# Performance work log

Measured on AMD Instinct MI355X. Metric: run time of the kernel, lower is better.

Reference implementation:

```python
import jax, jax.numpy as jnp
import numpy as np

B, C, L = 2, 2, 20
D = H = W = 160


def setup_inputs() -> dict:
    key = jax.random.key(0)
    k1, k2, k3, k4 = jax.random.split(key, 4)
    labels = jax.random.randint(k1, (B, 1, D, H, W), 0, L, dtype=jnp.int32)
    means = jax.random.normal(k2, (B, L, C), dtype=jnp.float32)
    stds = jax.random.uniform(k3, (B, L, C), dtype=jnp.float32)
    # noise is sampled once per (b, c) volume in the original module
    noise = jax.random.normal(k4, (B, C, D, H, W), dtype=jnp.float32)
    gen_labels = jnp.arange(L, dtype=jnp.int32)  # generation_labels (sorted)
    return {"labels": labels, "means": means, "stds": stds,
            "noise": noise, "gen_labels": gen_labels}


def reference(labels, means, stds, noise, gen_labels):
    Bb, _, Dd, Hh, Ww = labels.shape
    Cc = means.shape[-1]
    Ll = gen_labels.shape[0]
    lab = labels[:, 0].reshape(Bb, -1)                      # [B, V]
    # map label value -> index into generation_labels (sorted)
    idx = jnp.searchsorted(gen_labels, lab)                 # [B, V]
    idx = jnp.clip(idx, 0, Ll - 1)
    valid = gen_labels[idx] == lab                          # labels not in set stay 0
    m = jnp.take_along_axis(means, idx[:, :, None], axis=1)  # [B, V, C]
    s = jnp.take_along_axis(stds, idx[:, :, None], axis=1)   # [B, V, C]
    n = noise.reshape(Bb, Cc, -1).transpose(0, 2, 1)         # [B, V, C]
    out = jnp.where(valid[:, :, None], m + s * n, jnp.float32(0))
    return out.transpose(0, 2, 1).reshape(Bb, Cc, Dd, Hh, Ww)
```

## Files before the change

### kernel.cpp

```cpp
#include <hip/hip_runtime.h>


__device__ __forceinline__ int searchsorted_left(const int* __restrict__ g, int L, int x) {
    int lo = 0, hi = L;
    while (lo < hi) {
        int mid = (lo + hi) >> 1;
        if (g[mid] < x) lo = mid + 1; else hi = mid;
    }
    return lo;
}

__global__ __launch_bounds__(256) void gmm_sample_kernel(
    const int*   __restrict__ labels,
    const float* __restrict__ means,
    const float* __restrict__ stds,
    const float* __restrict__ noise,
    const int*   __restrict__ gen_labels,
    float*       __restrict__ out,
    int B, int L, int C, int V)
{
    extern __shared__ char smem_raw[];
    int*   sgl = (int*)smem_raw;
    float* sm  = (float*)(sgl + L);
    float* ss  = sm + B * L * C;

    const int BLC = B * L * C;
    for (int i = threadIdx.x; i < L;   i += blockDim.x) sgl[i] = gen_labels[i];
    for (int i = threadIdx.x; i < BLC; i += blockDim.x) { sm[i] = means[i]; ss[i] = stds[i]; }
    __syncthreads();

    const int NV4   = V >> 2;
    const int total = B * NV4;
    const int stride = gridDim.x * blockDim.x;

    for (int g = blockIdx.x * blockDim.x + threadIdx.x; g < total; g += stride) {
        const int b  = g / NV4;
        const int v4 = g - b * NV4;

        const int4 lab = ((const int4*)labels)[b * NV4 + v4];
        const int labv[4] = {lab.x, lab.y, lab.z, lab.w};

        int  idx[4];
        bool val[4];
#pragma unroll
        for (int j = 0; j < 4; ++j) {
            int lo = searchsorted_left(sgl, L, labv[j]);
            int ix = lo < (L - 1) ? lo : (L - 1);
            idx[j] = ix;
            val[j] = (sgl[ix] == labv[j]);
        }

        for (int c = 0; c < C; ++c) {
            const int plane = (b * C + c) * NV4 + v4;
            const float4 nz = ((const float4*)noise)[plane];
            const float nv[4] = {nz.x, nz.y, nz.z, nz.w};
            float ov[4];
#pragma unroll
            for (int j = 0; j < 4; ++j) {
                const int t = (b * L + idx[j]) * C + c;
                ov[j] = val[j] ? fmaf(ss[t], nv[j], sm[t]) : 0.0f;
            }
            float4 o = make_float4(ov[0], ov[1], ov[2], ov[3]);
            ((float4*)out)[plane] = o;
        }
    }
}

__global__ void gmm_sample_tail_kernel(
    const int*   __restrict__ labels,
    const float* __restrict__ means,
    const float* __restrict__ stds,
    const float* __restrict__ noise,
    const int*   __restrict__ gen_labels,
    float*       __restrict__ out,
    int B, int L, int C, int V, int vstart)
{
    const int tail   = V - vstart;
    const int total  = B * tail;
    const int stride = gridDim.x * blockDim.x;
    for (int g = blockIdx.x * blockDim.x + threadIdx.x; g < total; g += stride) {
        const int b = g / tail;
        const int v = vstart + (g - b * tail);
        const int labv = labels[b * V + v];
        int lo = 0, hi = L;
        while (lo < hi) { int mid = (lo + hi) >> 1; if (gen_labels[mid] < labv) lo = mid + 1; else hi = mid; }
        int ix = lo < (L - 1) ? lo : (L - 1);
        bool valid = (gen_labels[ix] == labv);
        for (int c = 0; c < C; ++c) {
            const int t = (b * L + ix) * C + c;
            const long long p = (long long)(b * C + c) * V + v;
            out[p] = valid ? fmaf(stds[t], noise[p], means[t]) : 0.0f;
        }
    }
}

extern "C" void kernel_launch(void* const* d_in, const int* in_sizes, int n_in,
                              void* d_out, int out_size, void* d_ws, size_t ws_size,
                              hipStream_t stream) {
    const int*   labels = (const int*)  d_in[0];
    const float* means  = (const float*)d_in[1];
    const float* stds   = (const float*)d_in[2];
    const float* noise  = (const float*)d_in[3];
    const int*   gl     = (const int*)  d_in[4];
    float*       out    = (float*)      d_out;

    const int L   = in_sizes[4];
    const int C   = in_sizes[3] / in_sizes[0];
    const int B   = in_sizes[1] / (L * C);
    const int V   = in_sizes[0] / B;

    const int NV4   = V >> 2;
    const int total = B * NV4;
    const int block = 256;
    int grid = (total + block - 1) / block;
    if (grid > 2048) grid = 2048;
    if (grid < 1) grid = 1;

    const size_t smem = (size_t)L * sizeof(int) + 2ull * B * L * C * sizeof(float);

    gmm_sample_kernel<<<grid, block, smem, stream>>>(
        labels, means, stds, noise, gl, out, B, L, C, V);

    const int vstart = NV4 << 2;
    if (vstart < V) {
        const int tail_total = B * (V - vstart);
        int tgrid = (tail_total + block - 1) / block;
        if (tgrid > 256) tgrid = 256;
        gmm_sample_tail_kernel<<<tgrid, block, 0, stream>>>(
            labels, means, stds, noise, gl, out, B, L, C, V, vstart);
    }
}
```

Before: 31.29 us.

## Add contiguous-label fast path with packed LDS table and nontemporal stores

The kernel now runs as a 2D grid with one batch per blockIdx.y and stages only that batch's means and stds in LDS. For C=2 they are packed into one float4 per label. When gen_labels are consecutive integers, the binary search becomes a single subtract and unsigned range check, and each label needs one float4 LDS read. Each thread handles two float4 chunks per iteration and writes with nontemporal stores. The aim is to remove the per-element search and scattered LDS reads, at the cost of a runtime arithmetic check and a generic fallback path.

```diff
diff --git a/kernel.cpp b/kernel.cpp
--- a/kernel.cpp
+++ b/kernel.cpp
@@ -1,5 +1,7 @@
 #include <hip/hip_runtime.h>
 
+
+typedef float f32x4 __attribute__((ext_vector_type(4)));
 
 __device__ __forceinline__ int searchsorted_left(const int* __restrict__ g, int L, int x) {
     int lo = 0, hi = L;
@@ -10,7 +12,7 @@
     return lo;
 }
 
-__global__ __launch_bounds__(256) void gmm_sample_kernel(
+__global__ __launch_bounds__(256) void gmm_fast_kernel(
     const int*   __restrict__ labels,
     const float* __restrict__ means,
     const float* __restrict__ stds,
@@ -19,49 +21,109 @@
     float*       __restrict__ out,
     int B, int L, int C, int V)
 {
+    const int b = blockIdx.y;
+
     extern __shared__ char smem_raw[];
-    int*   sgl = (int*)smem_raw;
-    float* sm  = (float*)(sgl + L);
-    float* ss  = sm + B * L * C;
+    int*  sgl   = (int*)smem_raw;
+    char* after = (char*)(sgl + ((L + 3) & ~3));
+    f32x4* tbl  = (f32x4*)after;
+    float* smn  = (float*)after;
+    float* ssd  = smn + L * C;
 
-    const int BLC = B * L * C;
-    for (int i = threadIdx.x; i < L;   i += blockDim.x) sgl[i] = gen_labels[i];
-    for (int i = threadIdx.x; i < BLC; i += blockDim.x) { sm[i] = means[i]; ss[i] = stds[i]; }
+    for (int i = threadIdx.x; i < L; i += blockDim.x) sgl[i] = gen_labels[i];
+    if (C == 2) {
+        for (int i = threadIdx.x; i < L; i += blockDim.x) {
+            const float* mp = means + ((long long)b * L + i) * 2;
+            const float* sp = stds  + ((long long)b * L + i) * 2;
+            f32x4 t; t.x = mp[0]; t.y = mp[1]; t.z = sp[0]; t.w = sp[1];
+            tbl[i] = t;
+        }
+    } else {
+        const long long base = (long long)b * L * C;
+        for (int i = threadIdx.x; i < L * C; i += blockDim.x) {
+            smn[i] = means[base + i];
+            ssd[i] = stds[base + i];
+        }
+    }
     __syncthreads();
 
-    const int NV4   = V >> 2;
-    const int total = B * NV4;
-    const int stride = gridDim.x * blockDim.x;
+    const int g0 = sgl[0];
+    bool ar = true;
+    for (int i = 1; i < L; ++i) ar = ar && (sgl[i] == g0 + i);
 
-    for (int g = blockIdx.x * blockDim.x + threadIdx.x; g < total; g += stride) {
-        const int b  = g / NV4;
-        const int v4 = g - b * NV4;
+    const int NV4 = V >> 2;
+    const unsigned uL = (unsigned)L;
+    const int4* lab4 = (const int4*)(labels + (long long)b * V);
 
-        const int4 lab = ((const int4*)labels)[b * NV4 + v4];
-        const int labv[4] = {lab.x, lab.y, lab.z, lab.w};
-
-        int  idx[4];
-        bool val[4];
+    if (ar && C == 2) {
+        const f32x4* nz0 = (const f32x4*)(noise + (long long)(b * C + 0) * V);
+        const f32x4* nz1 = (const f32x4*)(noise + (long long)(b * C + 1) * V);
+        f32x4* o0 = (f32x4*)(out + (long long)(b * C + 0) * V);
+        f32x4* o1 = (f32x4*)(out + (long long)(b * C + 1) * V);
+        const int step = blockDim.x * 2;
+        for (int base = blockIdx.x * step; base < NV4; base += gridDim.x * step) {
 #pragma unroll
-        for (int j = 0; j < 4; ++j) {
-            int lo = searchsorted_left(sgl, L, labv[j]);
-            int ix = lo < (L - 1) ? lo : (L - 1);
-            idx[j] = ix;
-            val[j] = (sgl[ix] == labv[j]);
+            for (int h = 0; h < 2; ++h) {
+                const int i0 = base + h * blockDim.x + threadIdx.x;
+                if (i0 >= NV4) continue;
+                const int4 la = lab4[i0];
+                const int lv[4] = {la.x, la.y, la.z, la.w};
+                f32x4 t[4];
+                bool  val[4];
+#pragma unroll
+                for (int j = 0; j < 4; ++j) {
+                    const unsigned d = (unsigned)(lv[j] - g0);
+                    val[j] = d < uL;
+                    const unsigned ix = val[j] ? d : (uL - 1u);
+                    t[j] = tbl[ix];
+                }
+                const f32x4 na = nz0[i0];
+                const f32x4 nb = nz1[i0];
+                f32x4 oa, ob;
+                oa.x = val[0] ? fmaf(t[0].z, na.x, t[0].x) : 0.f;
+                oa.y = val[1] ? fmaf(t[1].z, na.y, t[1].x) : 0.f;
+                oa.z = val[2] ? fmaf(t[2].z, na.z, t[2].x) : 0.f;
+                oa.w = val[3] ? fmaf(t[3].z, na.w, t[3].x) : 0.f;
+                ob.x = val[0] ? fmaf(t[0].w, nb.x, t[0].y) : 0.f;
+                ob.y = val[1] ? fmaf(t[1].w, nb.y, t[1].y) : 0.f;
+                ob.z = val[2] ? fmaf(t[2].w, nb.z, t[2].y) : 0.f;
+                ob.w = val[3] ? fmaf(t[3].w, nb.w, t[3].y) : 0.f;
+                __builtin_nontemporal_store(oa, &o0[i0]);
+                __builtin_nontemporal_store(ob, &o1[i0]);
+            }
         }
-
-        for (int c = 0; c < C; ++c) {
-            const int plane = (b * C + c) * NV4 + v4;
-            const float4 nz = ((const float4*)noise)[plane];
-            const float nv[4] = {nz.x, nz.y, nz.z, nz.w};
-            float ov[4];
+    } else {
+        const int step = blockDim.x * 2;
+        for (int base = blockIdx.x * step; base < NV4; base += gridDim.x * step) {
 #pragma unroll
-            for (int j = 0; j < 4; ++j) {
-                const int t = (b * L + idx[j]) * C + c;
-                ov[j] = val[j] ? fmaf(ss[t], nv[j], sm[t]) : 0.0f;
+            for (int h = 0; h < 2; ++h) {
+                const int i0 = base + h * blockDim.x + threadIdx.x;
+                if (i0 >= NV4) continue;
+                const int4 la = lab4[i0];
+                const int lv[4] = {la.x, la.y, la.z, la.w};
+                int  idx[4]; bool val[4];
+#pragma unroll
+                for (int j = 0; j < 4; ++j) {
+                    int lo = searchsorted_left(sgl, L, lv[j]);
+                    int ix = lo < (L - 1) ? lo : (L - 1);
+                    idx[j] = ix;
+                    val[j] = (sgl[ix] == lv[j]);
+                }
+                for (int c = 0; c < C; ++c) {
+                    const long long plane = ((long long)(b * C + c) * V) >> 2;
+                    const float4 nzv = ((const float4*)noise)[plane + i0];
+                    const float nv[4] = {nzv.x, nzv.y, nzv.z, nzv.w};
+                    f32x4 o;
+#pragma unroll
+                    for (int j = 0; j < 4; ++j) {
+                        const int t = idx[j] * C + c;
+                        float r = val[j] ? fmaf(ssd[t], nv[j], smn[t]) : 0.f;
+                        if (j == 0) o.x = r; else if (j == 1) o.y = r;
+                        else if (j == 2) o.z = r; else o.w = r;
+                    }
+                    __builtin_nontemporal_store(o, (f32x4*)out + plane + i0);
+                }
             }
-            float4 o = make_float4(ov[0], ov[1], ov[2], ov[3]);
-            ((float4*)out)[plane] = o;
         }
     }
 }
@@ -81,7 +143,7 @@
     for (int g = blockIdx.x * blockDim.x + threadIdx.x; g < total; g += stride) {
         const int b = g / tail;
         const int v = vstart + (g - b * tail);
-        const int labv = labels[b * V + v];
+        const int labv = labels[(long long)b * V + v];
         int lo = 0, hi = L;
         while (lo < hi) { int mid = (lo + hi) >> 1; if (gen_labels[mid] < labv) lo = mid + 1; else hi = mid; }
         int ix = lo < (L - 1) ? lo : (L - 1);
@@ -104,21 +166,25 @@
     const int*   gl     = (const int*)  d_in[4];
     float*       out    = (float*)      d_out;
 
-    const int L   = in_sizes[4];
-    const int C   = in_sizes[3] / in_sizes[0];
-    const int B   = in_sizes[1] / (L * C);
-    const int V   = in_sizes[0] / B;
+    const int L = in_sizes[4];
+    const int C = in_sizes[3] / in_sizes[0];
+    const int B = in_sizes[1] / (L * C);
+    const int V = in_sizes[0] / B;
 
-    const int NV4   = V >> 2;
-    const int total = B * NV4;
+    const int NV4  = V >> 2;
     const int block = 256;
-    int grid = (total + block - 1) / block;
-    if (grid > 2048) grid = 2048;
-    if (grid < 1) grid = 1;
+    const int per_block = block * 2;
+    int gx = (NV4 + per_block - 1) / per_block;
+    if (gx > 1024) gx = 1024;
+    if (gx < 1) gx = 1;
+    dim3 grid(gx, B);
 
-    const size_t smem = (size_t)L * sizeof(int) + 2ull * B * L * C * sizeof(float);
+    size_t tblBytes = (size_t)L * 16;
+    size_t genBytes = 2ull * L * C * sizeof(float);
+    size_t smem = (size_t)((L + 3) & ~3) * sizeof(int) +
+                  (tblBytes > genBytes ? tblBytes : genBytes);
 
-    gmm_sample_kernel<<<grid, block, smem, stream>>>(
+    gmm_fast_kernel<<<grid, block, smem, stream>>>(
         labels, means, stds, noise, gl, out, B, L, C, V);
 
     const int vstart = NV4 << 2;
```

New measurement: 30.72 us. About the same (-1.8%).
